# Kernel tuning notes

Measured on AMD Instinct MI355X. Metric: run time of the kernel, lower is better.

Reference implementation:

```python
import jax, jax.numpy as jnp
import numpy as np

N_NODES = 50000
N_EDGES = 1000000
NODE_DIM = 128
EDGE_DIM = 64


def setup_inputs() -> dict:
    key = jax.random.key(0)
    ks = jax.random.split(key, 12)
    s = 1.0 / np.sqrt(EDGE_DIM)
    sn = 1.0 / np.sqrt(NODE_DIM)
    return {
        "x": jax.random.normal(ks[0], (N_NODES, NODE_DIM), jnp.float32),
        "edge_index": jax.random.randint(ks[1], (2, N_EDGES), 0, N_NODES, jnp.int64),
        "edge_attr": jax.random.normal(ks[2], (N_EDGES, EDGE_DIM), jnp.float32),
        # lin_e: edge_dim -> edge_dim
        "We": jax.random.uniform(ks[3], (EDGE_DIM, EDGE_DIM), jnp.float32, -s, s),
        "be": jax.random.uniform(ks[4], (EDGE_DIM,), jnp.float32, -s, s),
        # lin_s: node_dim -> edge_dim
        "Ws": jax.random.uniform(ks[5], (EDGE_DIM, NODE_DIM), jnp.float32, -sn, sn),
        "bs": jax.random.uniform(ks[6], (EDGE_DIM,), jnp.float32, -sn, sn),
        # lin_t: node_dim -> edge_dim
        "Wt": jax.random.uniform(ks[7], (EDGE_DIM, NODE_DIM), jnp.float32, -sn, sn),
        "bt": jax.random.uniform(ks[8], (EDGE_DIM,), jnp.float32, -sn, sn),
        # lin1: edge_dim -> edge_dim
        "W1": jax.random.uniform(ks[9], (EDGE_DIM, EDGE_DIM), jnp.float32, -s, s),
        "b1": jax.random.uniform(ks[10], (EDGE_DIM,), jnp.float32, -s, s),
    }


def reference(x, edge_index, edge_attr, We, be, Ws, bs, Wt, bt, W1, b1):
    # node projections: [N, edge_dim]
    x_s = x @ Ws.T + bs
    x_t = x @ Wt.T + bt
    # fused edge update: lin_e(edge_attr) + gather(x_s, src) + gather(x_t, tgt)
    e = edge_attr @ We.T + be + x_s[edge_index[0]] + x_t[edge_index[1]]  # [E, edge_dim]
    e = jax.nn.gelu(e)
    return e @ W1.T + b1
```

## Files before the change

kernel.cpp:

```cpp
#include <hip/hip_runtime.h>
#include <stdint.h>

#define N_NODES_C 50000
#define N_EDGES_C 1000000
#define NODE_DIM_C 128
#define EDGE_DIM_C 64

typedef __attribute__((ext_vector_type(8))) short short8;
typedef __attribute__((ext_vector_type(4))) float floatx4;

__device__ __forceinline__ short f2bf(float f) {
    union { float f; uint32_t u; } v; v.f = f;
    uint32_t u = v.u;
    uint32_t r = (u + 0x7FFFu + ((u >> 16) & 1u)) >> 16;
    return (short)r;
}

__device__ __forceinline__ float gelu_tanh(float x) {
    float u = x * x;
    float inner = x * (1.0f + 0.044715f * u);
    float z = 1.5957691216057308f * inner;
    float ez = __expf(-z);
    return x / (1.0f + ez);
}

__global__ __launch_bounds__(256) void node_proj_kernel(
    const float* __restrict__ x,
    const float* __restrict__ Ws, const float* __restrict__ bs,
    const float* __restrict__ Wt, const float* __restrict__ bt,
    float* __restrict__ xs, float* __restrict__ xt)
{
    __shared__ __align__(16) short ws_frag[4][4][64][8];
    __shared__ __align__(16) short wt_frag[4][4][64][8];

    const int tid = threadIdx.x;
    for (int eidx = tid; eidx < 1024; eidx += 256) {
        int t = eidx >> 8;
        int s = (eidx >> 6) & 3;
        int l = eidx & 63;
        int n = t * 16 + (l & 15);
        int kb = s * 32 + ((l >> 4) << 3);
        const float* wsr = Ws + n * NODE_DIM_C + kb;
        const float* wtr = Wt + n * NODE_DIM_C + kb;
#pragma unroll
        for (int i = 0; i < 8; ++i) {
            ws_frag[t][s][l][i] = f2bf(wsr[i]);
            wt_frag[t][s][l][i] = f2bf(wtr[i]);
        }
    }
    __syncthreads();

    const int wave = tid >> 6, lane = tid & 63;
    const int m = lane & 15, q = lane >> 4;
    const int base = blockIdx.x * 64 + wave * 16;
    const int arow = base + m;

    floatx4 accS[4], accT[4];
    const floatx4 zero = {0.f, 0.f, 0.f, 0.f};
#pragma unroll
    for (int t = 0; t < 4; ++t) { accS[t] = zero; accT[t] = zero; }

#pragma unroll
    for (int s = 0; s < 4; ++s) {
        short8 a;
        if (arow < N_NODES_C) {
            const float4* ap = (const float4*)(x + arow * NODE_DIM_C + s * 32 + q * 8);
            float4 a0 = ap[0], a1 = ap[1];
            a[0] = f2bf(a0.x); a[1] = f2bf(a0.y); a[2] = f2bf(a0.z); a[3] = f2bf(a0.w);
            a[4] = f2bf(a1.x); a[5] = f2bf(a1.y); a[6] = f2bf(a1.z); a[7] = f2bf(a1.w);
        } else {
#pragma unroll
            for (int i = 0; i < 8; ++i) a[i] = 0;
        }
#pragma unroll
        for (int t = 0; t < 4; ++t) {
            short8 bS = *(const short8*)ws_frag[t][s][lane];
            short8 bT = *(const short8*)wt_frag[t][s][lane];
            accS[t] = __builtin_amdgcn_mfma_f32_16x16x32_bf16(a, bS, accS[t], 0, 0, 0);
            accT[t] = __builtin_amdgcn_mfma_f32_16x16x32_bf16(a, bT, accT[t], 0, 0, 0);
        }
    }

#pragma unroll
    for (int t = 0; t < 4; ++t) {
        int col = t * 16 + m;
        float bsv = bs[col], btv = bt[col];
#pragma unroll
        for (int r = 0; r < 4; ++r) {
            int n = base + q * 4 + r;
            if (n < N_NODES_C) {
                xs[n * EDGE_DIM_C + col] = accS[t][r] + bsv;
                xt[n * EDGE_DIM_C + col] = accT[t][r] + btv;
            }
        }
    }
}

__global__ __launch_bounds__(256) void edge_mlp_kernel(
    const float* __restrict__ ea, const int* __restrict__ ei,
    const float* __restrict__ We, const float* __restrict__ be,
    const float* __restrict__ W1, const float* __restrict__ b1,
    const float* __restrict__ xs, const float* __restrict__ xt,
    float* __restrict__ out)
{
    __shared__ __align__(16) short we_frag[4][2][64][8];
    __shared__ __align__(16) short w1_frag[4][2][64][8];
    __shared__ __align__(16) short pbuf[4][16][72];

    const int tid = threadIdx.x;
    for (int eidx = tid; eidx < 512; eidx += 256) {
        int t = eidx >> 7;
        int s = (eidx >> 6) & 1;
        int l = eidx & 63;
        int n = t * 16 + (l & 15);
        int kb = s * 32 + ((l >> 4) << 3);
        const float* wer = We + n * EDGE_DIM_C + kb;
        const float* w1r = W1 + n * EDGE_DIM_C + kb;
#pragma unroll
        for (int i = 0; i < 8; ++i) {
            we_frag[t][s][l][i] = f2bf(wer[i]);
            w1_frag[t][s][l][i] = f2bf(w1r[i]);
        }
    }
    __syncthreads();

    const int wave = tid >> 6, lane = tid & 63;
    const int m = lane & 15, q = lane >> 4;
    const int* __restrict__ src = ei;
    const int* __restrict__ tgt = ei + N_EDGES_C;

    float bev[4], b1v[4];
#pragma unroll
    for (int t = 0; t < 4; ++t) { bev[t] = be[t * 16 + m]; b1v[t] = b1[t * 16 + m]; }

    const floatx4 zero = {0.f, 0.f, 0.f, 0.f};
    const int nchunks = N_EDGES_C / 64;

    for (int chunk = blockIdx.x; chunk < nchunks; chunk += gridDim.x) {
        const int base = chunk * 64 + wave * 16;

        floatx4 acc[4];
#pragma unroll
        for (int t = 0; t < 4; ++t) acc[t] = zero;
#pragma unroll
        for (int s = 0; s < 2; ++s) {
            const float4* ap = (const float4*)(ea + (base + m) * EDGE_DIM_C + s * 32 + q * 8);
            float4 a0 = ap[0], a1 = ap[1];
            short8 a;
            a[0] = f2bf(a0.x); a[1] = f2bf(a0.y); a[2] = f2bf(a0.z); a[3] = f2bf(a0.w);
            a[4] = f2bf(a1.x); a[5] = f2bf(a1.y); a[6] = f2bf(a1.z); a[7] = f2bf(a1.w);
#pragma unroll
            for (int t = 0; t < 4; ++t) {
                short8 b = *(const short8*)we_frag[t][s][lane];
                acc[t] = __builtin_amdgcn_mfma_f32_16x16x32_bf16(a, b, acc[t], 0, 0, 0);
            }
        }

        int sidx[4], tidx[4];
#pragma unroll
        for (int r = 0; r < 4; ++r) {
            int e = base + q * 4 + r;
            int si = src[e], ti = tgt[e];
            sidx[r] = min(max(si, 0), N_NODES_C - 1);
            tidx[r] = min(max(ti, 0), N_NODES_C - 1);
        }
#pragma unroll
        for (int t = 0; t < 4; ++t) {
            int col = t * 16 + m;
#pragma unroll
            for (int r = 0; r < 4; ++r) {
                float c = acc[t][r] + bev[t]
                        + xs[sidx[r] * EDGE_DIM_C + col]
                        + xt[tidx[r] * EDGE_DIM_C + col];
                pbuf[wave][q * 4 + r][col] = f2bf(gelu_tanh(c));
            }
        }

        floatx4 acc2[4];
#pragma unroll
        for (int t = 0; t < 4; ++t) acc2[t] = zero;
#pragma unroll
        for (int s = 0; s < 2; ++s) {
            short8 a2 = *(const short8*)&pbuf[wave][m][s * 32 + q * 8];
#pragma unroll
            for (int t = 0; t < 4; ++t) {
                short8 b = *(const short8*)w1_frag[t][s][lane];
                acc2[t] = __builtin_amdgcn_mfma_f32_16x16x32_bf16(a2, b, acc2[t], 0, 0, 0);
            }
        }

#pragma unroll
        for (int t = 0; t < 4; ++t) {
            int col = t * 16 + m;
#pragma unroll
            for (int r = 0; r < 4; ++r) {
                int e = base + q * 4 + r;
                out[e * EDGE_DIM_C + col] = acc2[t][r] + b1v[t];
            }
        }
    }
}

extern "C" void kernel_launch(void* const* d_in, const int* in_sizes, int n_in,
                              void* d_out, int out_size, void* d_ws, size_t ws_size,
                              hipStream_t stream) {
    const float* x   = (const float*)d_in[0];
    const int*   ei  = (const int*)d_in[1];
    const float* ea  = (const float*)d_in[2];
    const float* We  = (const float*)d_in[3];
    const float* be  = (const float*)d_in[4];
    const float* Ws  = (const float*)d_in[5];
    const float* bs  = (const float*)d_in[6];
    const float* Wt  = (const float*)d_in[7];
    const float* bt  = (const float*)d_in[8];
    const float* W1  = (const float*)d_in[9];
    const float* b1  = (const float*)d_in[10];
    float* out = (float*)d_out;

    float* xs = (float*)d_ws;
    float* xt = xs + (size_t)N_NODES_C * EDGE_DIM_C;

    dim3 blk(256);
    dim3 grid_nodes((N_NODES_C + 63) / 64);
    node_proj_kernel<<<grid_nodes, blk, 0, stream>>>(x, Ws, bs, Wt, bt, xs, xt);

    dim3 grid_edges(3125);
    edge_mlp_kernel<<<grid_edges, blk, 0, stream>>>(ea, ei, We, be, W1, b1, xs, xt, out);
}
```

Baseline: 513.7 us.

## Issue all global loads before weight staging and launch one chunk per block

In both kernels, loads of the activation rows, edge indices, weights and gathered node projections are now issued before the shared-memory weight staging and barrier, so their latency overlaps with weight conversion. The edge kernel drops its grid-stride loop and launches one block per 64-edge chunk (15625 blocks). Weight loads are vectorised to float4 and packed into bf16 with single 16-byte shared stores. The cost is higher register pressure from the prefetched values, and each block now stages the weights for only one chunk.

Result: slower. 531.7 us (+3.5%).

```diff
diff --git a/kernel.cpp b/kernel.cpp
--- a/kernel.cpp
+++ b/kernel.cpp
@@ -14,6 +14,13 @@
     uint32_t u = v.u;
     uint32_t r = (u + 0x7FFFu + ((u >> 16) & 1u)) >> 16;
     return (short)r;
+}
+
+__device__ __forceinline__ short8 pack8(float4 a0, float4 a1) {
+    short8 o;
+    o[0] = f2bf(a0.x); o[1] = f2bf(a0.y); o[2] = f2bf(a0.z); o[3] = f2bf(a0.w);
+    o[4] = f2bf(a1.x); o[5] = f2bf(a1.y); o[6] = f2bf(a1.z); o[7] = f2bf(a1.w);
+    return o;
 }
 
 __device__ __forceinline__ float gelu_tanh(float x) {
@@ -34,26 +41,37 @@
     __shared__ __align__(16) short wt_frag[4][4][64][8];
 
     const int tid = threadIdx.x;
+    const int wave = tid >> 6, lane = tid & 63;
+    const int m = lane & 15, q = lane >> 4;
+    const int base = blockIdx.x * 64 + wave * 16;
+    const int arow = base + m;
+
+    float4 av[4][2];
+#pragma unroll
+    for (int s = 0; s < 4; ++s) {
+        if (arow < N_NODES_C) {
+            const float4* ap = (const float4*)(x + arow * NODE_DIM_C + s * 32 + q * 8);
+            av[s][0] = ap[0]; av[s][1] = ap[1];
+        } else {
+            av[s][0] = make_float4(0.f, 0.f, 0.f, 0.f);
+            av[s][1] = make_float4(0.f, 0.f, 0.f, 0.f);
+        }
+    }
+
     for (int eidx = tid; eidx < 1024; eidx += 256) {
         int t = eidx >> 8;
         int s = (eidx >> 6) & 3;
         int l = eidx & 63;
         int n = t * 16 + (l & 15);
         int kb = s * 32 + ((l >> 4) << 3);
-        const float* wsr = Ws + n * NODE_DIM_C + kb;
-        const float* wtr = Wt + n * NODE_DIM_C + kb;
-#pragma unroll
-        for (int i = 0; i < 8; ++i) {
-            ws_frag[t][s][l][i] = f2bf(wsr[i]);
-            wt_frag[t][s][l][i] = f2bf(wtr[i]);
-        }
+        const float4* wsr = (const float4*)(Ws + n * NODE_DIM_C + kb);
+        const float4* wtr = (const float4*)(Wt + n * NODE_DIM_C + kb);
+        float4 s0 = wsr[0], s1 = wsr[1];
+        float4 t0 = wtr[0], t1 = wtr[1];
+        *(short8*)ws_frag[t][s][l] = pack8(s0, s1);
+        *(short8*)wt_frag[t][s][l] = pack8(t0, t1);
     }
     __syncthreads();
-
-    const int wave = tid >> 6, lane = tid & 63;
-    const int m = lane & 15, q = lane >> 4;
-    const int base = blockIdx.x * 64 + wave * 16;
-    const int arow = base + m;
 
     floatx4 accS[4], accT[4];
     const floatx4 zero = {0.f, 0.f, 0.f, 0.f};
@@ -62,16 +80,7 @@
 
 #pragma unroll
     for (int s = 0; s < 4; ++s) {
-        short8 a;
-        if (arow < N_NODES_C) {
-            const float4* ap = (const float4*)(x + arow * NODE_DIM_C + s * 32 + q * 8);
-            float4 a0 = ap[0], a1 = ap[1];
-            a[0] = f2bf(a0.x); a[1] = f2bf(a0.y); a[2] = f2bf(a0.z); a[3] = f2bf(a0.w);
-            a[4] = f2bf(a1.x); a[5] = f2bf(a1.y); a[6] = f2bf(a1.z); a[7] = f2bf(a1.w);
-        } else {
-#pragma unroll
-            for (int i = 0; i < 8; ++i) a[i] = 0;
-        }
+        short8 a = pack8(av[s][0], av[s][1]);
 #pragma unroll
         for (int t = 0; t < 4; ++t) {
             short8 bS = *(const short8*)ws_frag[t][s][lane];
@@ -108,95 +117,114 @@
     __shared__ __align__(16) short pbuf[4][16][72];
 
     const int tid = threadIdx.x;
-    for (int eidx = tid; eidx < 512; eidx += 256) {
-        int t = eidx >> 7;
-        int s = (eidx >> 6) & 1;
-        int l = eidx & 63;
+    const int wave = tid >> 6, lane = tid & 63;
+    const int m = lane & 15, q = lane >> 4;
+    const int base = blockIdx.x * 64 + wave * 16;
+    const int* __restrict__ src = ei;
+    const int* __restrict__ tgt = ei + N_EDGES_C;
+
+    int sidx[4], tidx[4];
+#pragma unroll
+    for (int r = 0; r < 4; ++r) {
+        int e = base + q * 4 + r;
+        int si = src[e], ti = tgt[e];
+        sidx[r] = min(max(si, 0), N_NODES_C - 1);
+        tidx[r] = min(max(ti, 0), N_NODES_C - 1);
+    }
+
+    float4 av[4];
+#pragma unroll
+    for (int s = 0; s < 2; ++s) {
+        const float4* ap = (const float4*)(ea + (base + m) * EDGE_DIM_C + s * 32 + q * 8);
+        av[s * 2] = ap[0];
+        av[s * 2 + 1] = ap[1];
+    }
+
+    float4 web[2][2], w1b[2][2];
+#pragma unroll
+    for (int j = 0; j < 2; ++j) {
+        int eidx = tid + j * 256;
+        int t = eidx >> 7, s = (eidx >> 6) & 1, l = eidx & 63;
         int n = t * 16 + (l & 15);
         int kb = s * 32 + ((l >> 4) << 3);
-        const float* wer = We + n * EDGE_DIM_C + kb;
-        const float* w1r = W1 + n * EDGE_DIM_C + kb;
-#pragma unroll
-        for (int i = 0; i < 8; ++i) {
-            we_frag[t][s][l][i] = f2bf(wer[i]);
-            w1_frag[t][s][l][i] = f2bf(w1r[i]);
-        }
-    }
+        const float4* wer = (const float4*)(We + n * EDGE_DIM_C + kb);
+        const float4* w1r = (const float4*)(W1 + n * EDGE_DIM_C + kb);
+        web[j][0] = wer[0]; web[j][1] = wer[1];
+        w1b[j][0] = w1r[0]; w1b[j][1] = w1r[1];
+    }
+
+    float bev[4], b1v[4];
+#pragma unroll
+    for (int t = 0; t < 4; ++t) { bev[t] = be[t * 16 + m]; b1v[t] = b1[t * 16 + m]; }
+
+    float gxs[4][4], gxt[4][4];
+#pragma unroll
+    for (int r = 0; r < 4; ++r) {
+        const float* ps = xs + (size_t)sidx[r] * EDGE_DIM_C + m;
+        const float* pt = xt + (size_t)tidx[r] * EDGE_DIM_C + m;
+#pragma unroll
+        for (int t = 0; t < 4; ++t) {
+            gxs[r][t] = ps[t * 16];
+            gxt[r][t] = pt[t * 16];
+        }
+    }
+
+#pragma unroll
+    for (int j = 0; j < 2; ++j) {
+        int eidx = tid + j * 256;
+        int t = eidx >> 7, s = (eidx >> 6) & 1, l = eidx & 63;
+        *(short8*)we_frag[t][s][l] = pack8(web[j][0], web[j][1]);
+        *(short8*)w1_frag[t][s][l] = pack8(w1b[j][0], w1b[j][1]);
+    }
+
+    short8 af[2];
+#pragma unroll
+    for (int s = 0; s < 2; ++s) af[s] = pack8(av[s * 2], av[s * 2 + 1]);
+
     __syncthreads();
 
-    const int wave = tid >> 6, lane = tid & 63;
-    const int m = lane & 15, q = lane >> 4;
-    const int* __restrict__ src = ei;
-    const int* __restrict__ tgt = ei + N_EDGES_C;
-
-    float bev[4], b1v[4];
-#pragma unroll
-    for (int t = 0; t < 4; ++t) { bev[t] = be[t * 16 + m]; b1v[t] = b1[t * 16 + m]; }
-
     const floatx4 zero = {0.f, 0.f, 0.f, 0.f};
-    const int nchunks = N_EDGES_C / 64;
-
-    for (int chunk = blockIdx.x; chunk < nchunks; chunk += gridDim.x) {
-        const int base = chunk * 64 + wave * 16;
-
-        floatx4 acc[4];
-#pragma unroll
-        for (int t = 0; t < 4; ++t) acc[t] = zero;
-#pragma unroll
-        for (int s = 0; s < 2; ++s) {
-            const float4* ap = (const float4*)(ea + (base + m) * EDGE_DIM_C + s * 32 + q * 8);
-            float4 a0 = ap[0], a1 = ap[1];
-            short8 a;
-            a[0] = f2bf(a0.x); a[1] = f2bf(a0.y); a[2] = f2bf(a0.z); a[3] = f2bf(a0.w);
-            a[4] = f2bf(a1.x); a[5] = f2bf(a1.y); a[6] = f2bf(a1.z); a[7] = f2bf(a1.w);
-#pragma unroll
-            for (int t = 0; t < 4; ++t) {
-                short8 b = *(const short8*)we_frag[t][s][lane];
-                acc[t] = __builtin_amdgcn_mfma_f32_16x16x32_bf16(a, b, acc[t], 0, 0, 0);
-            }
-        }
-
-        int sidx[4], tidx[4];
+    floatx4 acc[4];
+#pragma unroll
+    for (int t = 0; t < 4; ++t) acc[t] = zero;
+#pragma unroll
+    for (int s = 0; s < 2; ++s) {
+#pragma unroll
+        for (int t = 0; t < 4; ++t) {
+            short8 b = *(const short8*)we_frag[t][s][lane];
+            acc[t] = __builtin_amdgcn_mfma_f32_16x16x32_bf16(af[s], b, acc[t], 0, 0, 0);
+        }
+    }
+
+#pragma unroll
+    for (int t = 0; t < 4; ++t) {
+#pragma unroll
+        for (int r = 0; r < 4; ++r) {
+            float c = acc[t][r] + bev[t] + gxs[r][t] + gxt[r][t];
+            pbuf[wave][q * 4 + r][t * 16 + m] = f2bf(gelu_tanh(c));
+        }
+    }
+
+    floatx4 acc2[4];
+#pragma unroll
+    for (int t = 0; t < 4; ++t) acc2[t] = zero;
+#pragma unroll
+    for (int s = 0; s < 2; ++s) {
+        short8 a2 = *(const short8*)&pbuf[wave][m][s * 32 + q * 8];
+#pragma unroll
+        for (int t = 0; t < 4; ++t) {
+            short8 b = *(const short8*)w1_frag[t][s][lane];
+            acc2[t] = __builtin_amdgcn_mfma_f32_16x16x32_bf16(a2, b, acc2[t], 0, 0, 0);
+        }
+    }
+
+#pragma unroll
+    for (int t = 0; t < 4; ++t) {
+        int col = t * 16 + m;
 #pragma unroll
         for (int r = 0; r < 4; ++r) {
             int e = base + q * 4 + r;
-            int si = src[e], ti = tgt[e];
-            sidx[r] = min(max(si, 0), N_NODES_C - 1);
-            tidx[r] = min(max(ti, 0), N_NODES_C - 1);
-        }
-#pragma unroll
-        for (int t = 0; t < 4; ++t) {
-            int col = t * 16 + m;
-#pragma unroll
-            for (int r = 0; r < 4; ++r) {
-                float c = acc[t][r] + bev[t]
-                        + xs[sidx[r] * EDGE_DIM_C + col]
-                        + xt[tidx[r] * EDGE_DIM_C + col];
-                pbuf[wave][q * 4 + r][col] = f2bf(gelu_tanh(c));
-            }
-        }
-
-        floatx4 acc2[4];
-#pragma unroll
-        for (int t = 0; t < 4; ++t) acc2[t] = zero;
-#pragma unroll
-        for (int s = 0; s < 2; ++s) {
-            short8 a2 = *(const short8*)&pbuf[wave][m][s * 32 + q * 8];
-#pragma unroll
-            for (int t = 0; t < 4; ++t) {
-                short8 b = *(const short8*)w1_frag[t][s][lane];
-                acc2[t] = __builtin_amdgcn_mfma_f32_16x16x32_bf16(a2, b, acc2[t], 0, 0, 0);
-            }
-        }
-
-#pragma unroll
-        for (int t = 0; t < 4; ++t) {
-            int col = t * 16 + m;
-#pragma unroll
-            for (int r = 0; r < 4; ++r) {
-                int e = base + q * 4 + r;
-                out[e * EDGE_DIM_C + col] = acc2[t][r] + b1v[t];
-            }
+            out[e * EDGE_DIM_C + col] = acc2[t][r] + b1v[t];
         }
     }
 }
@@ -224,6 +252,6 @@
     dim3 grid_nodes((N_NODES_C + 63) / 64);
     node_proj_kernel<<<grid_nodes, blk, 0, stream>>>(x, Ws, bs, Wt, bt, xs, xt);
 
-    dim3 grid_edges(3125);
+    dim3 grid_edges(N_EDGES_C / 64);
     edge_mlp_kernel<<<grid_edges, blk, 0, stream>>>(ea, ei, We, be, W1, b1, xs, xt, out);
 }
```
